# Kernel optimization log

Measured on AMD Instinct MI355X. Metric: run time of the kernel, lower is better.

## Reference

```python
import jax, jax.numpy as jnp
import numpy as np

B, T, D = 2, 4096, 512
H = 8  # heads; head_dim = D // H = 64


def setup_inputs() -> dict:
    key = jax.random.key(0)
    ks = jax.random.split(key, 8)
    s = 0.02
    return {
        "queries": jax.random.normal(ks[0], (B, T, D), jnp.float32),
        "keys": jax.random.normal(ks[1], (B, T, D), jnp.float32),
        "values": jax.random.normal(ks[2], (B, T, D), jnp.float32),
        "Wq": jax.random.normal(ks[3], (D, D), jnp.float32) * s,
        "Wk": jax.random.normal(ks[4], (D, D), jnp.float32) * s,
        "Wv": jax.random.normal(ks[5], (D, D), jnp.float32) * s,
        "Wo": jax.random.normal(ks[6], (D, D), jnp.float32) * s,
        "bo": jnp.zeros((D,), jnp.float32),
    }


def reference(queries, keys, values, Wq, Wk, Wv, Wo, bo):
    # pad_dim = 0 for in_dim=512, n_heads=8, so no padding needed.
    Bq, Tq, _ = queries.shape
    Ts = keys.shape[1]
    hd = D // H
    # torch Linear: x @ W.T
    q = (queries @ Wq.T).reshape(Bq, Tq, H, hd).transpose(0, 2, 1, 3)  # [B,H,T,hd]
    k = (keys @ Wk.T).reshape(Bq, Ts, H, hd).transpose(0, 2, 1, 3)
    v = (values @ Wv.T).reshape(Bq, Ts, H, hd).transpose(0, 2, 1, 3)
    attn = jnp.einsum("bhtd,bhsd->bhts", q, k) / np.sqrt(hd).astype(np.float32)
    attn = jax.nn.softmax(attn, axis=-1)  # [B,H,T,Ts]
    z = jnp.einsum("bhts,bhsd->bhtd", attn, v)
    z = z.transpose(0, 2, 1, 3).reshape(Bq, Tq, D)
    out = z @ Wo.T + bo
    return (out, attn)
```

## Files before the change

kernel.cpp:

```cpp
#include <hip/hip_runtime.h>

typedef __attribute__((ext_vector_type(8))) short bf16x8;
typedef __attribute__((ext_vector_type(8))) unsigned short u16x8;
typedef __attribute__((ext_vector_type(4))) float f32x4;
typedef __attribute__((ext_vector_type(2))) unsigned uint2v;

#define DEVINL __device__ __forceinline__

constexpr int TB = 2;
constexpr int TT = 4096;
constexpr int TD = 512;
constexpr int TH = 8;
constexpr int THD = 64;
constexpr int TM = TB * TT;

DEVINL unsigned short f2b(float f) {
  unsigned u = __builtin_bit_cast(unsigned, f);
  u += 0x7FFFu + ((u >> 16) & 1u);
  return (unsigned short)(u >> 16);
}

DEVINL unsigned cvtpk(float lo, float hi) {
  unsigned r;
  asm("v_cvt_pk_bf16_f32 %0, %1, %2" : "=v"(r) : "v"(lo), "v"(hi));
  return r;
}

DEVINL void lgkm_barrier() {
  asm volatile("s_waitcnt lgkmcnt(0)" ::: "memory");
  __builtin_amdgcn_s_barrier();
  __builtin_amdgcn_sched_barrier(0);
}

template<int MODE>
__global__ __launch_bounds__(256, 2)
void gemm_xwt(const float* __restrict__ X, const float* __restrict__ W,
              unsigned short* __restrict__ Yb, float* __restrict__ Yf,
              const float* __restrict__ bias)
{
  constexpr int K = TD, N = TD;
  __shared__ unsigned short As[128][72];
  __shared__ unsigned short Bs[128][72];

  const int t    = threadIdx.x;
  const int lane = t & 63, w = t >> 6;
  const int fr = lane & 15, fq = lane >> 4;
  const int wr = (w >> 1) * 64, wc = (w & 1) * 64;
  const int bm = blockIdx.x * 128, bn = blockIdx.y * 128;
  const int srow = t >> 1;
  const int skh  = (t & 1) * 32;

  f32x4 acc[4][4];
  #pragma unroll
  for (int i = 0; i < 4; ++i)
    #pragma unroll
    for (int j = 0; j < 4; ++j)
      acc[i][j] = f32x4{0.f, 0.f, 0.f, 0.f};

  for (int k0 = 0; k0 < K; k0 += 64) {
    const float* srcA = X + (size_t)(bm + srow) * K + k0 + skh;
    const float* srcB = W + (size_t)(bn + srow) * K + k0 + skh;
    #pragma unroll
    for (int i = 0; i < 4; ++i) {
      float4 a0 = ((const float4*)srcA)[2 * i];
      float4 a1 = ((const float4*)srcA)[2 * i + 1];
      u16x8 oa = {f2b(a0.x), f2b(a0.y), f2b(a0.z), f2b(a0.w),
                  f2b(a1.x), f2b(a1.y), f2b(a1.z), f2b(a1.w)};
      *(u16x8*)&As[srow][skh + i * 8] = oa;
      float4 b0 = ((const float4*)srcB)[2 * i];
      float4 b1 = ((const float4*)srcB)[2 * i + 1];
      u16x8 ob = {f2b(b0.x), f2b(b0.y), f2b(b0.z), f2b(b0.w),
                  f2b(b1.x), f2b(b1.y), f2b(b1.z), f2b(b1.w)};
      *(u16x8*)&Bs[srow][skh + i * 8] = ob;
    }
    __syncthreads();
    #pragma unroll
    for (int kk = 0; kk < 2; ++kk) {
      bf16x8 af[4], bfv[4];
      #pragma unroll
      for (int i = 0; i < 4; ++i)
        af[i] = *(const bf16x8*)&As[wr + i * 16 + fr][kk * 32 + fq * 8];
      #pragma unroll
      for (int j = 0; j < 4; ++j)
        bfv[j] = *(const bf16x8*)&Bs[wc + j * 16 + fr][kk * 32 + fq * 8];
      #pragma unroll
      for (int i = 0; i < 4; ++i)
        #pragma unroll
        for (int j = 0; j < 4; ++j) {
          if (MODE == 2)
            acc[i][j] = __builtin_amdgcn_mfma_f32_16x16x32_bf16(bfv[i], af[j], acc[i][j], 0, 0, 0);
          else
            acc[i][j] = __builtin_amdgcn_mfma_f32_16x16x32_bf16(af[i], bfv[j], acc[i][j], 0, 0, 0);
        }
    }
    __syncthreads();
  }

  #pragma unroll
  for (int i = 0; i < 4; ++i) {
    #pragma unroll
    for (int j = 0; j < 4; ++j) {
      #pragma unroll
      for (int ii = 0; ii < 4; ++ii) {
        float v = acc[i][j][ii];
        if (MODE == 2) {
          const int Nidx = bn + wc + i * 16 + fq * 4 + ii;
          const int Midx = bm + wr + j * 16 + fr;
          const int h = Nidx >> 6, d = Nidx & (THD - 1);
          const int b = Midx >> 12, tt = Midx & (TT - 1);
          Yb[((size_t)(b * TH + h) * THD + d) * TT + tt] = f2b(v);
        } else {
          const int gm = bm + wr + i * 16 + fq * 4 + ii;
          const int gn = bn + wc + j * 16 + fr;
          if (MODE == 1) Yf[(size_t)gm * N + gn] = v + bias[gn];
          else           Yb[(size_t)gm * N + gn] = f2b(v);
        }
      }
    }
  }
}

__global__ __launch_bounds__(256, 2)
void attn_fused(const unsigned short* __restrict__ Qb,
                const unsigned short* __restrict__ Kb,
                const unsigned short* __restrict__ VTg,
                float* __restrict__ attnO, float* __restrict__ Z)
{
  __shared__ unsigned short Ks[2][64][72];
  __shared__ unsigned short VTs[2][64][72];
  __shared__ unsigned short Ps[4][16][72];

  const int t    = threadIdx.x;
  const int lane = t & 63, w = t >> 6;
  const int fr = lane & 15, fq = lane >> 4;
  const int bh = blockIdx.y;
  const int b  = bh >> 3, h = bh & 7;
  const int q0 = blockIdx.x * 64;

  const size_t rowKV  = ((size_t)(b * TT)) * TD + h * THD;
  const size_t vtBase = (size_t)bh * THD * TT;

  const int tr = t >> 2;
  const int tc = (t & 3) * 16;

  auto loadK = [&](int kv0, u16x8& r0, u16x8& r1) {
    const unsigned short* src = Kb + rowKV + (size_t)(kv0 + tr) * TD + tc;
    r0 = *(const u16x8*)src;
    r1 = *(const u16x8*)(src + 8);
  };
  auto loadVT = [&](int kv0, u16x8& r0, u16x8& r1) {
    const unsigned short* src = VTg + vtBase + (size_t)tr * TT + kv0 + tc;
    r0 = *(const u16x8*)src;
    r1 = *(const u16x8*)(src + 8);
  };
  auto writeK = [&](int buf, const u16x8& r0, const u16x8& r1) {
    *(u16x8*)&Ks[buf][tr][tc]     = r0;
    *(u16x8*)&Ks[buf][tr][tc + 8] = r1;
  };
  auto writeVT = [&](int buf, const u16x8& r0, const u16x8& r1) {
    *(u16x8*)&VTs[buf][tr][tc]     = r0;
    *(u16x8*)&VTs[buf][tr][tc + 8] = r1;
  };

  const unsigned short* qsrc = Qb + ((size_t)(b * TT + q0 + w * 16 + fr)) * TD + h * THD;
  bf16x8 aq[2];
  aq[0] = *(const bf16x8*)(qsrc + fq * 8);
  aq[1] = *(const bf16x8*)(qsrc + 32 + fq * 8);

  constexpr int NT = TT / 64;
  constexpr float K2 = 0.18033688011112042f;

  u16x8 kr0, kr1, vr0, vr1;
  loadK(0, kr0, kr1);
  writeK(0, kr0, kr1);
  lgkm_barrier();

  float lsum = 0.f;
  for (int j = 0; j < NT; ++j) {
    const int cur = j & 1;
    if (j + 1 < NT) loadK((j + 1) * 64, kr0, kr1);
    __builtin_amdgcn_s_setprio(1);
    #pragma unroll
    for (int n = 0; n < 4; ++n) {
      f32x4 s = f32x4{0.f, 0.f, 0.f, 0.f};
      #pragma unroll
      for (int kk = 0; kk < 2; ++kk) {
        bf16x8 ak = *(const bf16x8*)&Ks[cur][n * 16 + fr][kk * 32 + fq * 8];
        s = __builtin_amdgcn_mfma_f32_16x16x32_bf16(ak, aq[kk], s, 0, 0, 0);
      }
      #pragma unroll
      for (int i = 0; i < 4; ++i)
        lsum += __builtin_amdgcn_exp2f(s[i] * K2);
    }
    __builtin_amdgcn_s_setprio(0);
    if (j + 1 < NT) writeK(cur ^ 1, kr0, kr1);
    lgkm_barrier();
  }
  lsum += __shfl_xor(lsum, 16, 64);
  lsum += __shfl_xor(lsum, 32, 64);
  const float l2i = -__log2f(lsum);

  loadK(0, kr0, kr1);
  loadVT(0, vr0, vr1);
  writeK(0, kr0, kr1);
  writeVT(0, vr0, vr1);
  lgkm_barrier();

  f32x4 accz[4];
  #pragma unroll
  for (int n = 0; n < 4; ++n) accz[n] = f32x4{0.f, 0.f, 0.f, 0.f};

  float* arow = attnO + ((size_t)bh * TT + q0 + w * 16 + fr) * TT + fq * 4;

  for (int j = 0; j < NT; ++j) {
    const int cur = j & 1;
    const int kv0 = j * 64;
    if (j + 1 < NT) {
      loadK((j + 1) * 64, kr0, kr1);
      loadVT((j + 1) * 64, vr0, vr1);
    }
    f32x4 sv[4];
    __builtin_amdgcn_s_setprio(1);
    #pragma unroll
    for (int n = 0; n < 4; ++n) {
      f32x4 s = f32x4{0.f, 0.f, 0.f, 0.f};
      #pragma unroll
      for (int kk = 0; kk < 2; ++kk) {
        bf16x8 ak = *(const bf16x8*)&Ks[cur][n * 16 + fr][kk * 32 + fq * 8];
        s = __builtin_amdgcn_mfma_f32_16x16x32_bf16(ak, aq[kk], s, 0, 0, 0);
      }
      sv[n] = s;
    }
    __builtin_amdgcn_s_setprio(0);
    float p[4][4];
    #pragma unroll
    for (int n = 0; n < 4; ++n)
      #pragma unroll
      for (int i = 0; i < 4; ++i)
        p[n][i] = __builtin_amdgcn_exp2f(fmaf(sv[n][i], K2, l2i));
    #pragma unroll
    for (int n = 0; n < 4; ++n) {
      f32x4 pv4 = {p[n][0], p[n][1], p[n][2], p[n][3]};
      __builtin_nontemporal_store(pv4, (f32x4*)(arow + kv0 + n * 16));
    }
    #pragma unroll
    for (int n = 0; n < 4; ++n) {
      uint2v u = {cvtpk(p[n][0], p[n][1]), cvtpk(p[n][2], p[n][3])};
      *(uint2v*)&Ps[w][fr][n * 16 + fq * 4] = u;
    }
    asm volatile("s_waitcnt lgkmcnt(0)" ::: "memory");
    __builtin_amdgcn_sched_barrier(0);
    __builtin_amdgcn_s_setprio(1);
    #pragma unroll
    for (int kk = 0; kk < 2; ++kk) {
      bf16x8 ap = *(const bf16x8*)&Ps[w][fr][kk * 32 + fq * 8];
      #pragma unroll
      for (int n = 0; n < 4; ++n) {
        bf16x8 bv = *(const bf16x8*)&VTs[cur][n * 16 + fr][kk * 32 + fq * 8];
        accz[n] = __builtin_amdgcn_mfma_f32_16x16x32_bf16(ap, bv, accz[n], 0, 0, 0);
      }
    }
    __builtin_amdgcn_s_setprio(0);
    if (j + 1 < NT) {
      writeK(cur ^ 1, kr0, kr1);
      writeVT(cur ^ 1, vr0, vr1);
    }
    lgkm_barrier();
  }

  const size_t zbase = ((size_t)(b * TT + q0 + w * 16 + fq * 4)) * TD + h * THD + fr;
  #pragma unroll
  for (int n = 0; n < 4; ++n)
    #pragma unroll
    for (int i = 0; i < 4; ++i)
      Z[zbase + (size_t)i * TD + n * 16] = accz[n][i];
}

extern "C" void kernel_launch(void* const* d_in, const int* in_sizes, int n_in,
                              void* d_out, int out_size, void* d_ws, size_t ws_size,
                              hipStream_t stream) {
  const float* queries = (const float*)d_in[0];
  const float* keys    = (const float*)d_in[1];
  const float* values  = (const float*)d_in[2];
  const float* Wq = (const float*)d_in[3];
  const float* Wk = (const float*)d_in[4];
  const float* Wv = (const float*)d_in[5];
  const float* Wo = (const float*)d_in[6];
  const float* bo = (const float*)d_in[7];

  float* out  = (float*)d_out;
  float* attn = out + (size_t)TM * TD;

  unsigned short* qb = (unsigned short*)d_ws;
  unsigned short* kb = qb + (size_t)TM * TD;
  unsigned short* vt = kb + (size_t)TM * TD;
  float*          zf = (float*)(vt + (size_t)TM * TD);

  dim3 gg(TM / 128, TD / 128), bb(256);
  gemm_xwt<0><<<gg, bb, 0, stream>>>(queries, Wq, qb, nullptr, nullptr);
  gemm_xwt<0><<<gg, bb, 0, stream>>>(keys,    Wk, kb, nullptr, nullptr);
  gemm_xwt<2><<<gg, bb, 0, stream>>>(values,  Wv, vt, nullptr, nullptr);

  attn_fused<<<dim3(TT / 64, TB * TH), bb, 0, stream>>>(qb, kb, vt, attn, zf);

  gemm_xwt<1><<<gg, bb, 0, stream>>>(zf, Wo, nullptr, out, bo);
}
```

Before: 534.4 us.

## Split KV across warps in attention block and keep P in registers

The fused attention kernel changes its work split. Instead of each warp owning 16 queries and looping over all 64 KV columns of a tile, each warp now owns 16 KV rows and computes scores for all 64 queries of the block. The bf16 probabilities stay in registers as MFMA A operands across two KV tiles, which removes the per-warp P tile round trip through shared memory and its waitcnt. V^T is staged in four buffers so two tiles can be consumed per PV step. In exchange, row sums and the Z accumulators must be reduced across warps through shared memory with extra barriers, and register pressure rises because each thread now holds a 4x4 set of accumulators.

```diff
diff --git a/kernel.cpp b/kernel.cpp
--- a/kernel.cpp
+++ b/kernel.cpp
@@ -4,6 +4,7 @@
 typedef __attribute__((ext_vector_type(8))) unsigned short u16x8;
 typedef __attribute__((ext_vector_type(4))) float f32x4;
 typedef __attribute__((ext_vector_type(2))) unsigned uint2v;
+typedef __attribute__((ext_vector_type(4))) unsigned uint4v;
 
 #define DEVINL __device__ __forceinline__
 
@@ -126,9 +127,11 @@
                 const unsigned short* __restrict__ VTg,
                 float* __restrict__ attnO, float* __restrict__ Z)
 {
-  __shared__ unsigned short Ks[2][64][72];
-  __shared__ unsigned short VTs[2][64][72];
-  __shared__ unsigned short Ps[4][16][72];
+  __shared__ __align__(16) char smem_[55552];
+  auto Ks   = (unsigned short (*)[64][72])smem_;
+  auto VTs  = (unsigned short (*)[64][72])(smem_ + 18432);
+  float* Lred = (float*)(smem_ + 55296);
+  auto Zs   = (float (*)[68])smem_;
 
   const int t    = threadIdx.x;
   const int lane = t & 63, w = t >> 6;
@@ -143,13 +146,13 @@
   const int tr = t >> 2;
   const int tc = (t & 3) * 16;
 
-  auto loadK = [&](int kv0, u16x8& r0, u16x8& r1) {
-    const unsigned short* src = Kb + rowKV + (size_t)(kv0 + tr) * TD + tc;
+  auto loadK = [&](int kvt, u16x8& r0, u16x8& r1) {
+    const unsigned short* src = Kb + rowKV + (size_t)(kvt * 64 + tr) * TD + tc;
     r0 = *(const u16x8*)src;
     r1 = *(const u16x8*)(src + 8);
   };
-  auto loadVT = [&](int kv0, u16x8& r0, u16x8& r1) {
-    const unsigned short* src = VTg + vtBase + (size_t)tr * TT + kv0 + tc;
+  auto loadVT = [&](int kvt, u16x8& r0, u16x8& r1) {
+    const unsigned short* src = VTg + vtBase + (size_t)tr * TT + kvt * 64 + tc;
     r0 = *(const u16x8*)src;
     r1 = *(const u16x8*)(src + 8);
   };
@@ -162,10 +165,14 @@
     *(u16x8*)&VTs[buf][tr][tc + 8] = r1;
   };
 
-  const unsigned short* qsrc = Qb + ((size_t)(b * TT + q0 + w * 16 + fr)) * TD + h * THD;
-  bf16x8 aq[2];
-  aq[0] = *(const bf16x8*)(qsrc + fq * 8);
-  aq[1] = *(const bf16x8*)(qsrc + 32 + fq * 8);
+  bf16x8 aq[4][2];
+  #pragma unroll
+  for (int qf = 0; qf < 4; ++qf) {
+    const unsigned short* qsrc =
+        Qb + ((size_t)(b * TT + q0 + qf * 16 + fr)) * TD + h * THD;
+    aq[qf][0] = *(const bf16x8*)(qsrc + fq * 8);
+    aq[qf][1] = *(const bf16x8*)(qsrc + 32 + fq * 8);
+  }
 
   constexpr int NT = TT / 64;
   constexpr float K2 = 0.18033688011112042f;
@@ -175,30 +182,44 @@
   writeK(0, kr0, kr1);
   lgkm_barrier();
 
-  float lsum = 0.f;
+  float lsum[4] = {0.f, 0.f, 0.f, 0.f};
   for (int j = 0; j < NT; ++j) {
     const int cur = j & 1;
-    if (j + 1 < NT) loadK((j + 1) * 64, kr0, kr1);
+    if (j + 1 < NT) loadK(j + 1, kr0, kr1);
+    bf16x8 ak0 = *(const bf16x8*)&Ks[cur][w * 16 + fr][fq * 8];
+    bf16x8 ak1 = *(const bf16x8*)&Ks[cur][w * 16 + fr][32 + fq * 8];
     __builtin_amdgcn_s_setprio(1);
     #pragma unroll
-    for (int n = 0; n < 4; ++n) {
+    for (int qf = 0; qf < 4; ++qf) {
       f32x4 s = f32x4{0.f, 0.f, 0.f, 0.f};
-      #pragma unroll
-      for (int kk = 0; kk < 2; ++kk) {
-        bf16x8 ak = *(const bf16x8*)&Ks[cur][n * 16 + fr][kk * 32 + fq * 8];
-        s = __builtin_amdgcn_mfma_f32_16x16x32_bf16(ak, aq[kk], s, 0, 0, 0);
-      }
+      s = __builtin_amdgcn_mfma_f32_16x16x32_bf16(ak0, aq[qf][0], s, 0, 0, 0);
+      s = __builtin_amdgcn_mfma_f32_16x16x32_bf16(ak1, aq[qf][1], s, 0, 0, 0);
       #pragma unroll
       for (int i = 0; i < 4; ++i)
-        lsum += __builtin_amdgcn_exp2f(s[i] * K2);
+        lsum[qf] += __builtin_amdgcn_exp2f(s[i] * K2);
     }
     __builtin_amdgcn_s_setprio(0);
     if (j + 1 < NT) writeK(cur ^ 1, kr0, kr1);
     lgkm_barrier();
   }
-  lsum += __shfl_xor(lsum, 16, 64);
-  lsum += __shfl_xor(lsum, 32, 64);
-  const float l2i = -__log2f(lsum);
+  #pragma unroll
+  for (int qf = 0; qf < 4; ++qf) {
+    lsum[qf] += __shfl_xor(lsum[qf], 16, 64);
+    lsum[qf] += __shfl_xor(lsum[qf], 32, 64);
+  }
+  if (fq == 0) {
+    #pragma unroll
+    for (int qf = 0; qf < 4; ++qf)
+      Lred[(w * 4 + qf) * 16 + fr] = lsum[qf];
+  }
+  __syncthreads();
+  float l2i[4];
+  #pragma unroll
+  for (int qf = 0; qf < 4; ++qf) {
+    float s = Lred[(0 * 4 + qf) * 16 + fr] + Lred[(1 * 4 + qf) * 16 + fr] +
+              Lred[(2 * 4 + qf) * 16 + fr] + Lred[(3 * 4 + qf) * 16 + fr];
+    l2i[qf] = -__log2f(s);
+  }
 
   loadK(0, kr0, kr1);
   loadVT(0, vr0, vr1);
@@ -206,74 +227,97 @@
   writeVT(0, vr0, vr1);
   lgkm_barrier();
 
-  f32x4 accz[4];
-  #pragma unroll
-  for (int n = 0; n < 4; ++n) accz[n] = f32x4{0.f, 0.f, 0.f, 0.f};
-
-  float* arow = attnO + ((size_t)bh * TT + q0 + w * 16 + fr) * TT + fq * 4;
-
-  for (int j = 0; j < NT; ++j) {
-    const int cur = j & 1;
-    const int kv0 = j * 64;
-    if (j + 1 < NT) {
-      loadK((j + 1) * 64, kr0, kr1);
-      loadVT((j + 1) * 64, vr0, vr1);
-    }
-    f32x4 sv[4];
+  f32x4 accz[4][4];
+  #pragma unroll
+  for (int i = 0; i < 4; ++i)
+    #pragma unroll
+    for (int j = 0; j < 4; ++j)
+      accz[i][j] = f32x4{0.f, 0.f, 0.f, 0.f};
+
+  unsigned pa[4][4];
+
+#define QK_TILE(J, HALF)                                                       \
+  {                                                                            \
+    if ((J) + 1 < NT) { loadK((J) + 1, kr0, kr1); loadVT((J) + 1, vr0, vr1); } \
+    bf16x8 ak0 = *(const bf16x8*)&Ks[(J) & 1][w * 16 + fr][fq * 8];            \
+    bf16x8 ak1 = *(const bf16x8*)&Ks[(J) & 1][w * 16 + fr][32 + fq * 8];       \
+    __builtin_amdgcn_s_setprio(1);                                             \
+    _Pragma("unroll")                                                          \
+    for (int qf = 0; qf < 4; ++qf) {                                           \
+      f32x4 s = f32x4{0.f, 0.f, 0.f, 0.f};                                     \
+      s = __builtin_amdgcn_mfma_f32_16x16x32_bf16(ak0, aq[qf][0], s, 0, 0, 0); \
+      s = __builtin_amdgcn_mfma_f32_16x16x32_bf16(ak1, aq[qf][1], s, 0, 0, 0); \
+      float p0 = __builtin_amdgcn_exp2f(fmaf(s[0], K2, l2i[qf]));              \
+      float p1 = __builtin_amdgcn_exp2f(fmaf(s[1], K2, l2i[qf]));              \
+      float p2 = __builtin_amdgcn_exp2f(fmaf(s[2], K2, l2i[qf]));              \
+      float p3 = __builtin_amdgcn_exp2f(fmaf(s[3], K2, l2i[qf]));              \
+      f32x4 pv4 = {p0, p1, p2, p3};                                            \
+      __builtin_nontemporal_store(pv4,                                         \
+        (f32x4*)(attnO + ((size_t)bh * TT + q0 + qf * 16 + fr) * TT            \
+                 + (J) * 64 + w * 16 + fq * 4));                               \
+      pa[qf][(HALF) * 2 + 0] = cvtpk(p0, p1);                                  \
+      pa[qf][(HALF) * 2 + 1] = cvtpk(p2, p3);                                  \
+    }                                                                          \
+    __builtin_amdgcn_s_setprio(0);                                             \
+  }
+#define STAGE_TAIL(J)                                                          \
+  {                                                                            \
+    if ((J) + 1 < NT) {                                                        \
+      writeK(((J) + 1) & 1, kr0, kr1);                                         \
+      writeVT(((J) + 1) & 3, vr0, vr1);                                        \
+    }                                                                          \
+    lgkm_barrier();                                                            \
+  }
+
+  for (int jp = 0; jp < NT / 2; ++jp) {
+    const int j0 = jp * 2;
+    const int vb = (jp & 1) * 2;
+    QK_TILE(j0, 0)
+    STAGE_TAIL(j0)
+    QK_TILE(j0 + 1, 1)
     __builtin_amdgcn_s_setprio(1);
     #pragma unroll
-    for (int n = 0; n < 4; ++n) {
-      f32x4 s = f32x4{0.f, 0.f, 0.f, 0.f};
-      #pragma unroll
-      for (int kk = 0; kk < 2; ++kk) {
-        bf16x8 ak = *(const bf16x8*)&Ks[cur][n * 16 + fr][kk * 32 + fq * 8];
-        s = __builtin_amdgcn_mfma_f32_16x16x32_bf16(ak, aq[kk], s, 0, 0, 0);
+    for (int df = 0; df < 4; ++df) {
+      uint2v lo = *(const uint2v*)&VTs[vb][df * 16 + fr][w * 16 + fq * 4];
+      uint2v hi = *(const uint2v*)&VTs[vb + 1][df * 16 + fr][w * 16 + fq * 4];
+      uint4v bvv = {lo[0], lo[1], hi[0], hi[1]};
+      bf16x8 bv = __builtin_bit_cast(bf16x8, bvv);
+      #pragma unroll
+      for (int qf = 0; qf < 4; ++qf) {
+        uint4v pav = {pa[qf][0], pa[qf][1], pa[qf][2], pa[qf][3]};
+        accz[qf][df] = __builtin_amdgcn_mfma_f32_16x16x32_bf16(
+            __builtin_bit_cast(bf16x8, pav), bv, accz[qf][df], 0, 0, 0);
       }
-      sv[n] = s;
     }
     __builtin_amdgcn_s_setprio(0);
-    float p[4][4];
-    #pragma unroll
-    for (int n = 0; n < 4; ++n)
-      #pragma unroll
-      for (int i = 0; i < 4; ++i)
-        p[n][i] = __builtin_amdgcn_exp2f(fmaf(sv[n][i], K2, l2i));
-    #pragma unroll
-    for (int n = 0; n < 4; ++n) {
-      f32x4 pv4 = {p[n][0], p[n][1], p[n][2], p[n][3]};
-      __builtin_nontemporal_store(pv4, (f32x4*)(arow + kv0 + n * 16));
-    }
-    #pragma unroll
-    for (int n = 0; n < 4; ++n) {
-      uint2v u = {cvtpk(p[n][0], p[n][1]), cvtpk(p[n][2], p[n][3])};
-      *(uint2v*)&Ps[w][fr][n * 16 + fq * 4] = u;
-    }
-    asm volatile("s_waitcnt lgkmcnt(0)" ::: "memory");
-    __builtin_amdgcn_sched_barrier(0);
-    __builtin_amdgcn_s_setprio(1);
-    #pragma unroll
-    for (int kk = 0; kk < 2; ++kk) {
-      bf16x8 ap = *(const bf16x8*)&Ps[w][fr][kk * 32 + fq * 8];
-      #pragma unroll
-      for (int n = 0; n < 4; ++n) {
-        bf16x8 bv = *(const bf16x8*)&VTs[cur][n * 16 + fr][kk * 32 + fq * 8];
-        accz[n] = __builtin_amdgcn_mfma_f32_16x16x32_bf16(ap, bv, accz[n], 0, 0, 0);
-      }
-    }
-    __builtin_amdgcn_s_setprio(0);
-    if (j + 1 < NT) {
-      writeK(cur ^ 1, kr0, kr1);
-      writeVT(cur ^ 1, vr0, vr1);
-    }
-    lgkm_barrier();
-  }
-
-  const size_t zbase = ((size_t)(b * TT + q0 + w * 16 + fq * 4)) * TD + h * THD + fr;
-  #pragma unroll
-  for (int n = 0; n < 4; ++n)
+    STAGE_TAIL(j0 + 1)
+  }
+#undef QK_TILE
+#undef STAGE_TAIL
+
+  for (int ww = 0; ww < 4; ++ww) {
+    if (w == ww) {
+      #pragma unroll
+      for (int qf = 0; qf < 4; ++qf)
+        #pragma unroll
+        for (int df = 0; df < 4; ++df)
+          #pragma unroll
+          for (int i = 0; i < 4; ++i) {
+            float* zp = &Zs[qf * 16 + fq * 4 + i][df * 16 + fr];
+            float v = accz[qf][df][i];
+            if (ww != 0) v += *zp;
+            *zp = v;
+          }
+    }
+    __syncthreads();
+  }
+  {
+    const int r = t >> 2, c4 = (t & 3) * 16;
+    float* zdst = Z + (size_t)(b * TT + q0 + r) * TD + h * THD + c4;
     #pragma unroll
     for (int i = 0; i < 4; ++i)
-      Z[zbase + (size_t)i * TD + n * 16] = accz[n][i];
+      *(f32x4*)(zdst + i * 4) = *(const f32x4*)&Zs[r][c4 + i * 4];
+  }
 }
 
 extern "C" void kernel_launch(void* const* d_in, const int* in_sizes, int n_in,
```

New measurement: 542.9 us. No clear change (+1.6%).
